# Performance work log

Hardware: AMD Instinct MI355X
Metric: run time of the kernel (lower is better)

Reference implementation:

```python
import jax, jax.numpy as jnp
import numpy as np

N, DIM = 4096, 1024

def setup_inputs() -> dict:
    key = jax.random.key(0)
    ks = jax.random.split(key, 5)
    scale = 1.0 / np.sqrt(DIM)
    return {
        "x": jax.random.normal(ks[0], (N, DIM), dtype=jnp.float32),
        "Wq": jax.random.normal(ks[1], (DIM, DIM), dtype=jnp.float32) * scale,
        "bq": jax.random.normal(ks[2], (DIM,), dtype=jnp.float32) * 0.01,
        "Wk": jax.random.normal(ks[3], (DIM, DIM), dtype=jnp.float32) * scale,
        "bk": jax.random.normal(ks[4], (DIM,), dtype=jnp.float32) * 0.01,
    }

def reference(x, Wq, bq, Wk, bk):
    # torch nn.Linear: y = x @ W.T + b
    q = x @ Wq.T + bq            # [N, D]
    k = x @ Wk.T + bk            # [N, D]
    scores = q @ k.T             # [N, N] (no 1/sqrt(d) scaling, as in source)
    attn = jax.nn.softmax(scores, axis=-1)
    return attn @ x              # weighted pooling over raw x (no value proj)
```

## Files before the change

### kernel.cpp

```cpp
#include <hip/hip_runtime.h>
#include <hip/hip_bf16.h>
#include <hip/hip_fp16.h>
#include <stdint.h>


using half8   = __attribute__((ext_vector_type(8))) _Float16;
using float4v = __attribute__((ext_vector_type(4))) float;
using int4v   = __attribute__((ext_vector_type(4))) int;
using uint2v  = __attribute__((ext_vector_type(2))) unsigned int;

#define QS        (6.0f / 32768.0f)
#define INV_S     (32768.0f / 6.0f)
#define INV_S256  (128.0f / 6.0f)
#define C_HH      (65536.0f * QS * QS)
#define C_X       (256.0f * QS * QS)

#define SX        (6.0f / 32768.0f)
#define SW        (0.25f / 32768.0f)
#define P_HH      (65536.0f * SX * SW)
#define P_X       (256.0f * SX * SW)

#define GLOAD_LDS16(gptr, ldsptr)                                              \
  __builtin_amdgcn_global_load_lds(                                            \
      (__attribute__((address_space(1))) void*)(uintptr_t)(gptr),              \
      (__attribute__((address_space(3))) void*)(unsigned)(uintptr_t)(ldsptr),  \
      16, 0, 0)

__device__ __forceinline__ void barrier_raw() {
  asm volatile("" ::: "memory");
  __builtin_amdgcn_s_barrier();
  asm volatile("" ::: "memory");
}

__device__ __forceinline__ int swz3(int row) {
  return (((row >> 2) & 3) << 1) ^ (row & 3);
}

__global__ __launch_bounds__(256, 2) void gemm_s_stats(
    const int8_t* __restrict__ Ahi, const int8_t* __restrict__ Alo,
    const int8_t* __restrict__ Bhi, const int8_t* __restrict__ Blo,
    _Float16* __restrict__ E, float2* __restrict__ stats)
{
  __shared__ __align__(16) int8_t smem[65536];
  int8_t* sAh = smem;
  int8_t* sAl = smem + 16384;
  int8_t* sBh = smem + 32768;
  int8_t* sBl = smem + 49152;

  const int tid  = threadIdx.x;
  const int wave = tid >> 6;
  const int lane = tid & 63;
  const int quad = lane >> 4;
  const int t16  = lane & 15;
  const int wm   = wave & 1;
  const int wn   = wave >> 1;
  const int row0 = blockIdx.y * 128;
  const int col0 = blockIdx.x * 128;

  const int seg  = lane & 3;
  const int rsub = lane >> 2;

  const int offA0 = (row0 + wave * 16 + rsub) * 2048 + seg * 16;
  const int offA1 = offA0 + 64 * 2048;
  const int offB0 = (col0 + wave * 16 + rsub) * 2048 + seg * 16;
  const int offB1 = offB0 + 64 * 2048;
  const int ldsT0 = (wave * 16) * 64;
  const int ldsT1 = (64 + wave * 16) * 64;

  int4v hh[4][4], cc[4][4];
#pragma unroll
  for (int i = 0; i < 4; ++i)
#pragma unroll
    for (int j = 0; j < 4; ++j) {
      hh[i][j] = (int4v){0, 0, 0, 0};
      cc[i][j] = (int4v){0, 0, 0, 0};
    }

  auto stage_AhBh = [&](int ks, int b) {
    const int k0 = ks * 64;
    GLOAD_LDS16(Ahi + offA0 + k0, sAh + b * 8192 + ldsT0);
    GLOAD_LDS16(Ahi + offA1 + k0, sAh + b * 8192 + ldsT1);
    GLOAD_LDS16(Bhi + offB0 + k0, sBh + b * 8192 + ldsT0);
    GLOAD_LDS16(Bhi + offB1 + k0, sBh + b * 8192 + ldsT1);
  };
  auto stage_Bl = [&](int ks, int b) {
    const int k0 = ks * 64;
    GLOAD_LDS16(Blo + offB0 + k0, sBl + b * 8192 + ldsT0);
    GLOAD_LDS16(Blo + offB1 + k0, sBl + b * 8192 + ldsT1);
  };
  auto stage_Al = [&](int ks, int b) {
    const int k0 = ks * 64;
    GLOAD_LDS16(Alo + offA0 + k0, sAl + b * 8192 + ldsT0);
    GLOAD_LDS16(Alo + offA1 + k0, sAl + b * 8192 + ldsT1);
  };

  stage_AhBh(0, 0);
  stage_Bl(0, 0);
  stage_Al(0, 0);

  int buf = 0;
  for (int ks = 0; ks < 16; ++ks) {
    asm volatile("s_waitcnt vmcnt(4)" ::: "memory");
    barrier_raw();
    if (ks < 15) stage_AhBh(ks + 1, buf ^ 1);

    int4v ah[4], bh[4];
#pragma unroll
    for (int i = 0; i < 4; ++i)
      ah[i] = *(const int4v*)(sAh + buf * 8192 +
                              (wm * 64 + i * 16 + t16) * 64 + quad * 16);
#pragma unroll
    for (int j = 0; j < 4; ++j)
      bh[j] = *(const int4v*)(sBh + buf * 8192 +
                              (wn * 64 + j * 16 + t16) * 64 + quad * 16);

    __builtin_amdgcn_s_setprio(1);
#pragma unroll
    for (int i = 0; i < 4; ++i)
#pragma unroll
      for (int j = 0; j < 4; ++j)
        hh[i][j] = __builtin_amdgcn_mfma_i32_16x16x64_i8(ah[i], bh[j], hh[i][j], 0, 0, 0);
    __builtin_amdgcn_s_setprio(0);

    if (ks < 15) asm volatile("s_waitcnt vmcnt(6)" ::: "memory");
    else         asm volatile("s_waitcnt vmcnt(2)" ::: "memory");
    barrier_raw();
    if (ks < 15) stage_Bl(ks + 1, buf ^ 1);

    int4v bl[4];
#pragma unroll
    for (int j = 0; j < 4; ++j)
      bl[j] = *(const int4v*)(sBl + buf * 8192 +
                              (wn * 64 + j * 16 + t16) * 64 + quad * 16);

    __builtin_amdgcn_s_setprio(1);
#pragma unroll
    for (int i = 0; i < 4; ++i)
#pragma unroll
      for (int j = 0; j < 4; ++j)
        cc[i][j] = __builtin_amdgcn_mfma_i32_16x16x64_i8(ah[i], bl[j], cc[i][j], 0, 0, 0);
    __builtin_amdgcn_s_setprio(0);

    if (ks < 15) asm volatile("s_waitcnt vmcnt(6)" ::: "memory");
    else         asm volatile("s_waitcnt vmcnt(0)" ::: "memory");
    barrier_raw();
    if (ks < 15) stage_Al(ks + 1, buf ^ 1);

    int4v al[4];
#pragma unroll
    for (int i = 0; i < 4; ++i)
      al[i] = *(const int4v*)(sAl + buf * 8192 +
                              (wm * 64 + i * 16 + t16) * 64 + quad * 16);

    __builtin_amdgcn_s_setprio(1);
#pragma unroll
    for (int i = 0; i < 4; ++i)
#pragma unroll
      for (int j = 0; j < 4; ++j)
        cc[i][j] = __builtin_amdgcn_mfma_i32_16x16x64_i8(al[i], bh[j], cc[i][j], 0, 0, 0);
    __builtin_amdgcn_s_setprio(0);

    buf ^= 1;
  }

  float* red = (float*)smem;

  float vv[4][4][4];
  float rmax[4][4];
#pragma unroll
  for (int i = 0; i < 4; ++i)
#pragma unroll
    for (int r = 0; r < 4; ++r) {
      float mx = -3.0e38f;
#pragma unroll
      for (int j = 0; j < 4; ++j) {
        float v = C_HH * (float)hh[i][j][r] + C_X * (float)cc[i][j][r];
        vv[i][j][r] = v;
        mx = fmaxf(mx, v);
      }
      mx = fmaxf(mx, __shfl_xor(mx, 1));
      mx = fmaxf(mx, __shfl_xor(mx, 2));
      mx = fmaxf(mx, __shfl_xor(mx, 4));
      mx = fmaxf(mx, __shfl_xor(mx, 8));
      rmax[i][r] = mx;
    }
  if (t16 == 0) {
#pragma unroll
    for (int i = 0; i < 4; ++i)
#pragma unroll
      for (int r = 0; r < 4; ++r)
        red[wn * 128 + wm * 64 + i * 16 + quad * 4 + r] = rmax[i][r];
  }
  __syncthreads();

  float mrow[4][4];
#pragma unroll
  for (int i = 0; i < 4; ++i)
#pragma unroll
    for (int r = 0; r < 4; ++r) {
      const int row = wm * 64 + i * 16 + quad * 4 + r;
      mrow[i][r] = fmaxf(red[row], red[128 + row]);
    }

  float rsum[4][4];
#pragma unroll
  for (int i = 0; i < 4; ++i)
#pragma unroll
    for (int r = 0; r < 4; ++r) {
      float s = 0.f;
#pragma unroll
      for (int j = 0; j < 4; ++j) {
        float e = __expf(vv[i][j][r] - mrow[i][r]);
        vv[i][j][r] = e;
        s += e;
      }
      s += __shfl_xor(s, 1);
      s += __shfl_xor(s, 2);
      s += __shfl_xor(s, 4);
      s += __shfl_xor(s, 8);
      rsum[i][r] = s;
    }
  if (t16 == 0) {
#pragma unroll
    for (int i = 0; i < 4; ++i)
#pragma unroll
      for (int r = 0; r < 4; ++r)
        red[256 + wn * 128 + wm * 64 + i * 16 + quad * 4 + r] = rsum[i][r];
  }

  uint16_t* img = (uint16_t*)(smem + 32768);
#pragma unroll
  for (int i = 0; i < 4; ++i)
#pragma unroll
    for (int j = 0; j < 4; ++j)
#pragma unroll
      for (int r = 0; r < 4; ++r) {
        const int row  = wm * 64 + i * 16 + quad * 4 + r;
        const int col  = wn * 64 + j * 16 + t16;
        const int colS = col ^ (((quad << 1) ^ r) << 3);
        _Float16 h = (_Float16)vv[i][j][r];
        img[row * 128 + colS] = *(const uint16_t*)&h;
      }
  __syncthreads();

#pragma unroll
  for (int it = 0; it < 8; ++it) {
    const int row    = wave * 32 + it * 4 + quad;
    const int chunkS = t16 ^ swz3(row);
    int4v v = *(const int4v*)&img[row * 128 + chunkS * 8];
    *(int4v*)&E[(size_t)(row0 + row) * 4096 + col0 + t16 * 8] = v;
  }

  if (wn == 0 && t16 == 0) {
#pragma unroll
    for (int i = 0; i < 4; ++i)
#pragma unroll
      for (int r = 0; r < 4; ++r) {
        const int row = wm * 64 + i * 16 + quad * 4 + r;
        const float l = red[256 + row] + red[256 + 128 + row];
        stats[(size_t)(row0 + row) * 32 + blockIdx.x] =
            make_float2(mrow[i][r], l);
      }
  }
}

__global__ __launch_bounds__(256, 2) void gemm_proj_i8(
    const int8_t* __restrict__ Ahi, const int8_t* __restrict__ Alo,
    const int8_t* __restrict__ Bhi, const int8_t* __restrict__ Blo,
    const float* __restrict__ biasQ, const float* __restrict__ biasK,
    int8_t* __restrict__ Ch, int8_t* __restrict__ Cl)
{
  __shared__ __align__(16) int8_t smem[65536];
  int8_t* sAh = smem;
  int8_t* sAl = smem + 16384;
  int8_t* sBh = smem + 32768;
  int8_t* sBl = smem + 49152;

  const int tid  = threadIdx.x;
  const int wave = tid >> 6;
  const int lane = tid & 63;
  const int quad = lane >> 4;
  const int t16  = lane & 15;
  const int wm   = wave & 1;
  const int wn   = wave >> 1;
  const int row0 = blockIdx.y * 128;
  const int col0 = blockIdx.x * 128;

  const int seg  = lane & 3;
  const int rsub = lane >> 2;

  const int offA0 = (row0 + wave * 16 + rsub) * 1024 + seg * 16;
  const int offA1 = offA0 + 64 * 1024;
  const int offB0 = (col0 + wave * 16 + rsub) * 1024 + seg * 16;
  const int offB1 = offB0 + 64 * 1024;
  const int ldsT0 = (wave * 16) * 64;
  const int ldsT1 = (64 + wave * 16) * 64;

  int4v hh[4][4], cc[4][4];
#pragma unroll
  for (int i = 0; i < 4; ++i)
#pragma unroll
    for (int j = 0; j < 4; ++j) {
      hh[i][j] = (int4v){0, 0, 0, 0};
      cc[i][j] = (int4v){0, 0, 0, 0};
    }

  auto stage_AhBh = [&](int ks, int b) {
    const int k0 = ks * 64;
    GLOAD_LDS16(Ahi + offA0 + k0, sAh + b * 8192 + ldsT0);
    GLOAD_LDS16(Ahi + offA1 + k0, sAh + b * 8192 + ldsT1);
    GLOAD_LDS16(Bhi + offB0 + k0, sBh + b * 8192 + ldsT0);
    GLOAD_LDS16(Bhi + offB1 + k0, sBh + b * 8192 + ldsT1);
  };
  auto stage_Bl = [&](int ks, int b) {
    const int k0 = ks * 64;
    GLOAD_LDS16(Blo + offB0 + k0, sBl + b * 8192 + ldsT0);
    GLOAD_LDS16(Blo + offB1 + k0, sBl + b * 8192 + ldsT1);
  };
  auto stage_Al = [&](int ks, int b) {
    const int k0 = ks * 64;
    GLOAD_LDS16(Alo + offA0 + k0, sAl + b * 8192 + ldsT0);
    GLOAD_LDS16(Alo + offA1 + k0, sAl + b * 8192 + ldsT1);
  };

  stage_AhBh(0, 0);
  stage_Bl(0, 0);
  stage_Al(0, 0);

  int buf = 0;
  for (int ks = 0; ks < 16; ++ks) {
    asm volatile("s_waitcnt vmcnt(4)" ::: "memory");
    barrier_raw();
    if (ks < 15) stage_AhBh(ks + 1, buf ^ 1);

    int4v ah[4], bh[4];
#pragma unroll
    for (int i = 0; i < 4; ++i)
      ah[i] = *(const int4v*)(sAh + buf * 8192 +
                              (wm * 64 + i * 16 + t16) * 64 + quad * 16);
#pragma unroll
    for (int j = 0; j < 4; ++j)
      bh[j] = *(const int4v*)(sBh + buf * 8192 +
                              (wn * 64 + j * 16 + t16) * 64 + quad * 16);

    __builtin_amdgcn_s_setprio(1);
#pragma unroll
    for (int i = 0; i < 4; ++i)
#pragma unroll
      for (int j = 0; j < 4; ++j)
        hh[i][j] = __builtin_amdgcn_mfma_i32_16x16x64_i8(ah[i], bh[j], hh[i][j], 0, 0, 0);
    __builtin_amdgcn_s_setprio(0);

    if (ks < 15) asm volatile("s_waitcnt vmcnt(6)" ::: "memory");
    else         asm volatile("s_waitcnt vmcnt(2)" ::: "memory");
    barrier_raw();
    if (ks < 15) stage_Bl(ks + 1, buf ^ 1);

    int4v bl[4];
#pragma unroll
    for (int j = 0; j < 4; ++j)
      bl[j] = *(const int4v*)(sBl + buf * 8192 +
                              (wn * 64 + j * 16 + t16) * 64 + quad * 16);

    __builtin_amdgcn_s_setprio(1);
#pragma unroll
    for (int i = 0; i < 4; ++i)
#pragma unroll
      for (int j = 0; j < 4; ++j)
        cc[i][j] = __builtin_amdgcn_mfma_i32_16x16x64_i8(ah[i], bl[j], cc[i][j], 0, 0, 0);
    __builtin_amdgcn_s_setprio(0);

    if (ks < 15) asm volatile("s_waitcnt vmcnt(6)" ::: "memory");
    else         asm volatile("s_waitcnt vmcnt(0)" ::: "memory");
    barrier_raw();
    if (ks < 15) stage_Al(ks + 1, buf ^ 1);

    int4v al[4];
#pragma unroll
    for (int i = 0; i < 4; ++i)
      al[i] = *(const int4v*)(sAl + buf * 8192 +
                              (wm * 64 + i * 16 + t16) * 64 + quad * 16);

    __builtin_amdgcn_s_setprio(1);
#pragma unroll
    for (int i = 0; i < 4; ++i)
#pragma unroll
      for (int j = 0; j < 4; ++j)
        cc[i][j] = __builtin_amdgcn_mfma_i32_16x16x64_i8(al[i], bh[j], cc[i][j], 0, 0, 0);
    __builtin_amdgcn_s_setprio(0);

    buf ^= 1;
  }

  uint16_t* img = (uint16_t*)(smem + 32768);
#pragma unroll
  for (int i = 0; i < 4; ++i) {
#pragma unroll
    for (int j = 0; j < 4; ++j) {
      const int ccol = col0 + wn * 64 + j * 16 + t16;
      const float* bp = (ccol < 1024) ? biasQ : (biasK - 1024);
#pragma unroll
      for (int r = 0; r < 4; ++r) {
        float v = P_HH * (float)hh[i][j][r] + P_X * (float)cc[i][j][r] + bp[ccol];
        int hi = (int)lrintf(v * INV_S256);
        hi = hi > 127 ? 127 : (hi < -127 ? -127 : hi);
        int lo = (int)lrintf(v * INV_S - 256.0f * (float)hi);
        lo = lo > 127 ? 127 : (lo < -127 ? -127 : lo);
        const int row  = wm * 64 + i * 16 + quad * 4 + r;
        const int col  = wn * 64 + j * 16 + t16;
        const int colS = col ^ (((quad << 1) ^ r) << 3);
        img[row * 128 + colS] = (uint16_t)((hi & 0xff) | ((lo & 0xff) << 8));
      }
    }
  }
  __syncthreads();

#pragma unroll
  for (int it = 0; it < 8; ++it) {
    const int row    = wave * 32 + it * 4 + quad;
    const int chunkS = t16 ^ swz3(row);
    int4v p = *(const int4v*)&img[row * 128 + chunkS * 8];
    const unsigned w0 = (unsigned)p[0], w1 = (unsigned)p[1];
    const unsigned w2 = (unsigned)p[2], w3 = (unsigned)p[3];
    uint2v hw, lw;
    hw[0] = (w0 & 0xffu) | (((w0 >> 16) & 0xffu) << 8) |
            ((w1 & 0xffu) << 16) | (((w1 >> 16) & 0xffu) << 24);
    hw[1] = (w2 & 0xffu) | (((w2 >> 16) & 0xffu) << 8) |
            ((w3 & 0xffu) << 16) | (((w3 >> 16) & 0xffu) << 24);
    lw[0] = ((w0 >> 8) & 0xffu) | (((w0 >> 24) & 0xffu) << 8) |
            (((w1 >> 8) & 0xffu) << 16) | ((w1 >> 24) << 24);
    lw[1] = ((w2 >> 8) & 0xffu) | (((w2 >> 24) & 0xffu) << 8) |
            (((w3 >> 8) & 0xffu) << 16) | ((w3 >> 24) << 24);
    const size_t go = (size_t)(row0 + row) * 2048 + col0 + t16 * 8;
    *(uint2v*)&Ch[go] = hw;
    *(uint2v*)&Cl[go] = lw;
  }
}

__global__ __launch_bounds__(512) void gemm_av(
    const uint16_t* __restrict__ E, const uint16_t* __restrict__ B,
    const float2* __restrict__ stats, float* __restrict__ out)
{
  __shared__ __align__(16) uint16_t stg[2][2][16384];
  __shared__ float betaS[128 * 33];

  const int L      = blockIdx.x;
  const int xcd    = L & 7;
  const int rest   = L >> 3;
  const int colb   = rest & 7;
  const int bandHi = rest >> 3;
  const int band   = xcd + 8 * bandHi;
  const int row0   = band * 128;
  const int col0   = colb * 128;

  const int tid  = threadIdx.x;
  const int wave = tid >> 6;
  const int z    = wave >> 2;
  const int gw   = wave & 3;
  const int lane = tid & 63;
  const int quad = lane >> 4;
  const int t16  = lane & 15;
  const int wm   = gw & 1;
  const int wn   = gw >> 1;

  const int c8   = lane & 7;
  const int r8   = lane >> 3;
  const int srcC = (c8 - r8) & 7;

  int offA[4], offB[4];
#pragma unroll
  for (int r = 0; r < 4; ++r) {
    offA[r] = (row0 + r * 32 + gw * 8 + r8) * 4096 + srcC * 8;
    offB[r] = (col0 + r * 32 + gw * 8 + r8) * 4096 + srcC * 8;
  }

  auto stage_s = [&](int s, int b) {
    const int k0h = (z * 16 + (s >> 1)) * 128 + (s & 1) * 64;
    uint16_t* sA = &stg[b][z][0];
    uint16_t* sB = &stg[b][z][8192];
#pragma unroll
    for (int r = 0; r < 4; ++r) {
      GLOAD_LDS16(E + offA[r] + k0h, &sA[(r * 32 + gw * 8) * 64]);
      GLOAD_LDS16(B + offB[r] + k0h, &sB[(r * 32 + gw * 8) * 64]);
    }
  };

  stage_s(0, 0);

  if (tid < 128) {
    const int row = row0 + tid;
    float2 st[32];
    float m = -3.0e38f;
#pragma unroll
    for (int t = 0; t < 32; ++t) {
      st[t] = stats[(size_t)row * 32 + t];
      m = fmaxf(m, st[t].x);
    }
    float l = 0.f;
#pragma unroll
    for (int t = 0; t < 32; ++t) l += st[t].y * __expf(st[t].x - m);
    const float inv = 1.0f / l;
#pragma unroll
    for (int t = 0; t < 32; ++t)
      betaS[tid * 33 + t] = __expf(st[t].x - m) * inv;
  }
  asm volatile("s_waitcnt vmcnt(0)" ::: "memory");
  __syncthreads();

  float4v acc[4][4];
#pragma unroll
  for (int i = 0; i < 4; ++i)
#pragma unroll
    for (int j = 0; j < 4; ++j)
      acc[i][j] = (float4v){0.f, 0.f, 0.f, 0.f};

  int buf = 0;
  for (int s = 0; s < 32; ++s) {
    if (s < 31) stage_s(s + 1, buf ^ 1);

    const int t = z * 16 + (s >> 1);
    _Float16 bb[4];
#pragma unroll
    for (int i = 0; i < 4; ++i)
      bb[i] = (_Float16)betaS[(wm * 64 + i * 16 + t16) * 33 + t];

    const uint16_t* sA = &stg[buf][z][0];
    const uint16_t* sB = &stg[buf][z][8192];

    half8 af[2][4], bf[2][4];
#pragma unroll
    for (int ks = 0; ks < 2; ++ks) {
#pragma unroll
      for (int i = 0; i < 4; ++i) {
        const int row = wm * 64 + i * 16 + t16;
        const int ch  = (ks * 4 + quad + (t16 & 7)) & 7;
        af[ks][i] = *(const half8*)&sA[row * 64 + ch * 8];
        half8 bs;
#pragma unroll
        for (int c = 0; c < 8; ++c) bs[c] = bb[i];
        af[ks][i] = af[ks][i] * bs;
      }
#pragma unroll
      for (int j = 0; j < 4; ++j) {
        const int row = wn * 64 + j * 16 + t16;
        const int ch  = (ks * 4 + quad + (t16 & 7)) & 7;
        bf[ks][j] = *(const half8*)&sB[row * 64 + ch * 8];
      }
    }

    __builtin_amdgcn_s_setprio(1);
#pragma unroll
    for (int ks = 0; ks < 2; ++ks)
#pragma unroll
      for (int i = 0; i < 4; ++i)
#pragma unroll
        for (int j = 0; j < 4; ++j)
          acc[i][j] = __builtin_amdgcn_mfma_f32_16x16x32_f16(af[ks][i], bf[ks][j], acc[i][j], 0, 0, 0);
    __builtin_amdgcn_s_setprio(0);

    if (s < 31) asm volatile("s_waitcnt vmcnt(0)" ::: "memory");
    barrier_raw();
    buf ^= 1;
  }

  float* xfer = (float*)stg;
#pragma unroll
  for (int h = 0; h < 2; ++h) {
    if (z == 1) {
#pragma unroll
      for (int i = 2 * h; i < 2 * h + 2; ++i)
#pragma unroll
        for (int j = 0; j < 4; ++j)
#pragma unroll
          for (int r = 0; r < 4; ++r) {
            const int e = (i - 2 * h) * 16 + j * 4 + r;
            xfer[e * 256 + gw * 64 + lane] = acc[i][j][r];
          }
    }
    __syncthreads();
    if (z == 0) {
#pragma unroll
      for (int i = 2 * h; i < 2 * h + 2; ++i)
#pragma unroll
        for (int j = 0; j < 4; ++j)
#pragma unroll
          for (int r = 0; r < 4; ++r) {
            const int e = (i - 2 * h) * 16 + j * 4 + r;
            acc[i][j][r] += xfer[e * 256 + gw * 64 + lane];
          }
    }
    __syncthreads();
  }

  float* img = (float*)((int8_t*)stg + 65536);
  if (z == 0) {
#pragma unroll
    for (int i = 0; i < 4; ++i)
#pragma unroll
      for (int j = 0; j < 4; ++j)
#pragma unroll
        for (int r = 0; r < 4; ++r) {
          const int row  = wm * 64 + i * 16 + quad * 4 + r;
          const int col  = wn * 64 + j * 16 + t16;
          const int colS = col ^ (((quad << 1) ^ r) << 2);
          img[row * 128 + colS] = acc[i][j][r];
        }
  }
  __syncthreads();

#pragma unroll
  for (int it = 0; it < 8; ++it) {
    const int row    = wave * 16 + (lane >> 2);
    const int chunk  = (lane & 3) * 8 + it;
    const int chunkS = chunk ^ swz3(row);
    float4v v = *(const float4v*)&img[row * 128 + chunkS * 4];
    *(float4v*)&out[(size_t)(row0 + row) * 1024 + col0 + chunk * 4] = v;
  }
}

__global__ __launch_bounds__(256) void quantT(
    const float* __restrict__ x, const float* __restrict__ Wq,
    const float* __restrict__ Wk,
    int8_t* __restrict__ xhi, int8_t* __restrict__ xlo,
    int8_t* __restrict__ whi, int8_t* __restrict__ wlo,
    uint16_t* __restrict__ xT)
{
  if (blockIdx.x < 6144) {
    int i = blockIdx.x * 256 + threadIdx.x;
    const float* src; int8_t* dh; int8_t* dl; int idx; float s256, s;
    if (i < 1048576)      { src = x;  idx = i;           dh = xhi; dl = xlo;
                            s256 = INV_S256; s = INV_S; }
    else if (i < 1310720) { src = Wq; idx = i - 1048576; dh = whi; dl = wlo;
                            s256 = 512.0f; s = 131072.0f; }
    else                  { src = Wk; idx = i - 1310720; dh = whi + 1048576;
                            dl = wlo + 1048576; s256 = 512.0f; s = 131072.0f; }
    float4 v = ((const float4*)src)[idx];
    float vv[4] = {v.x, v.y, v.z, v.w};
    int hp = 0, lp = 0;
#pragma unroll
    for (int c = 0; c < 4; ++c) {
      int h = (int)lrintf(vv[c] * s256);
      h = h > 127 ? 127 : (h < -127 ? -127 : h);
      int l = (int)lrintf(vv[c] * s - 256.0f * (float)h);
      l = l > 127 ? 127 : (l < -127 ? -127 : l);
      hp |= (h & 0xff) << (8 * c);
      lp |= (l & 0xff) << (8 * c);
    }
    ((int*)dh)[idx] = hp;
    ((int*)dl)[idx] = lp;
  } else {
    __shared__ float tile[32][33];
    const int tb = blockIdx.x - 6144;
    const int bx = tb & 31;
    const int by = tb >> 5;
    const int tx = threadIdx.x & 31;
    const int ty = threadIdx.x >> 5;
#pragma unroll
    for (int p = 0; p < 4; ++p) {
      const int row = by * 32 + ty + p * 8;
      tile[ty + p * 8][tx] = x[(size_t)row * 1024 + bx * 32 + tx];
    }
    __syncthreads();
#pragma unroll
    for (int p = 0; p < 4; ++p) {
      const int oc = ty + p * 8;
      __half hv = __float2half_rn(tile[tx][oc]);
      xT[(size_t)(bx * 32 + oc) * 4096 + by * 32 + tx] = *(uint16_t*)&hv;
    }
  }
}

extern "C" void kernel_launch(void* const* d_in, const int* in_sizes, int n_in,
                              void* d_out, int out_size, void* d_ws, size_t ws_size,
                              hipStream_t stream) {
  const int N = 4096, D = 1024;
  const float* x  = (const float*)d_in[0];
  const float* Wq = (const float*)d_in[1];
  const float* bq = (const float*)d_in[2];
  const float* Wk = (const float*)d_in[3];
  const float* bk = (const float*)d_in[4];
  float* out = (float*)d_out;

  char* w = (char*)d_ws;
  const size_t MiB = 1024 * 1024;
  int8_t*    xq_hi  = (int8_t*)   (w + 0  * MiB);
  int8_t*    xq_lo  = (int8_t*)   (w + 4  * MiB);
  int8_t*    Wqk_hi = (int8_t*)   (w + 8  * MiB);
  int8_t*    Wqk_lo = (int8_t*)   (w + 10 * MiB);
  int8_t*    qk_hi  = (int8_t*)   (w + 12 * MiB);
  int8_t*    qk_lo  = (int8_t*)   (w + 20 * MiB);
  _Float16*  E      = (_Float16*) (w + 36 * MiB);
  float2*    stats  = (float2*)   (w + 68 * MiB);
  uint16_t*  xTh    = (uint16_t*) (w + 72 * MiB);

  quantT<<<10240, 256, 0, stream>>>(x, Wq, Wk, xq_hi, xq_lo, Wqk_hi, Wqk_lo,
                                    xTh);

  gemm_proj_i8<<<dim3(2048 / 128, N / 128), 256, 0, stream>>>(
      xq_hi, xq_lo, Wqk_hi, Wqk_lo, bq, bk, qk_hi, qk_lo);

  gemm_s_stats<<<dim3(N / 128, N / 128), 256, 0, stream>>>(
      qk_hi, qk_lo, qk_hi + 1024, qk_lo + 1024, E, stats);

  gemm_av<<<256, 512, 0, stream>>>((const uint16_t*)E, xTh, stats, out);

  (void)in_sizes; (void)n_in; (void)out_size; (void)ws_size;
}
```

Baseline: 215.2 us.

## Replace split-K gemm_av with 128x64 tiles over 512 blocks of 256 threads

The attention-times-x GEMM drops its two-way split-K within a 512-thread block and instead uses 128x64 output tiles, giving 512 blocks of 256 threads with launch bounds allowing two blocks per CU. This removes the LDS cross-wave reduction and its extra barriers, and the smaller shared-memory footprint plus betaS stored as fp16 should let more blocks run at once. In exchange, each block reloads the full 128-row A strip for only 64 output columns, so global traffic for E roughly doubles, and the K loop is twice as long.

```diff
diff --git a/kernel.cpp b/kernel.cpp
--- a/kernel.cpp
+++ b/kernel.cpp
@@ -437,52 +437,52 @@
   }
 }
 
-__global__ __launch_bounds__(512) void gemm_av(
+__global__ __launch_bounds__(256, 2) void gemm_av(
     const uint16_t* __restrict__ E, const uint16_t* __restrict__ B,
     const float2* __restrict__ stats, float* __restrict__ out)
 {
-  __shared__ __align__(16) uint16_t stg[2][2][16384];
-  __shared__ float betaS[128 * 33];
+  __shared__ __align__(16) uint16_t stg[2][12288];
+  __shared__ _Float16 betaS[128 * 33];
 
   const int L      = blockIdx.x;
   const int xcd    = L & 7;
   const int rest   = L >> 3;
-  const int colb   = rest & 7;
-  const int bandHi = rest >> 3;
+  const int colb   = rest & 15;
+  const int bandHi = rest >> 4;
   const int band   = xcd + 8 * bandHi;
   const int row0   = band * 128;
-  const int col0   = colb * 128;
+  const int col0   = colb * 64;
 
   const int tid  = threadIdx.x;
   const int wave = tid >> 6;
-  const int z    = wave >> 2;
-  const int gw   = wave & 3;
   const int lane = tid & 63;
   const int quad = lane >> 4;
   const int t16  = lane & 15;
-  const int wm   = gw & 1;
-  const int wn   = gw >> 1;
-
+  const int wm   = wave & 1;
+  const int wn   = wave >> 1;
+
+  const int r8   = lane >> 3;
   const int c8   = lane & 7;
-  const int r8   = lane >> 3;
   const int srcC = (c8 - r8) & 7;
 
-  int offA[4], offB[4];
-#pragma unroll
-  for (int r = 0; r < 4; ++r) {
-    offA[r] = (row0 + r * 32 + gw * 8 + r8) * 4096 + srcC * 8;
-    offB[r] = (col0 + r * 32 + gw * 8 + r8) * 4096 + srcC * 8;
-  }
+  int offA[4], offBx[2];
+#pragma unroll
+  for (int p = 0; p < 4; ++p)
+    offA[p] = (row0 + p * 32 + wave * 8 + r8) * 4096 + srcC * 8;
+#pragma unroll
+  for (int p = 0; p < 2; ++p)
+    offBx[p] = (col0 + p * 32 + wave * 8 + r8) * 4096 + srcC * 8;
 
   auto stage_s = [&](int s, int b) {
-    const int k0h = (z * 16 + (s >> 1)) * 128 + (s & 1) * 64;
-    uint16_t* sA = &stg[b][z][0];
-    uint16_t* sB = &stg[b][z][8192];
-#pragma unroll
-    for (int r = 0; r < 4; ++r) {
-      GLOAD_LDS16(E + offA[r] + k0h, &sA[(r * 32 + gw * 8) * 64]);
-      GLOAD_LDS16(B + offB[r] + k0h, &sB[(r * 32 + gw * 8) * 64]);
-    }
+    const int k0h = s * 64;
+    uint16_t* sA = &stg[b][0];
+    uint16_t* sB = &stg[b][8192];
+#pragma unroll
+    for (int p = 0; p < 4; ++p)
+      GLOAD_LDS16(E + offA[p] + k0h, &sA[(p * 32 + wave * 8) * 64]);
+#pragma unroll
+    for (int p = 0; p < 2; ++p)
+      GLOAD_LDS16(B + offBx[p] + k0h, &sB[(p * 32 + wave * 8) * 64]);
   };
 
   stage_s(0, 0);
@@ -502,32 +502,32 @@
     const float inv = 1.0f / l;
 #pragma unroll
     for (int t = 0; t < 32; ++t)
-      betaS[tid * 33 + t] = __expf(st[t].x - m) * inv;
+      betaS[tid * 33 + t] = (_Float16)(__expf(st[t].x - m) * inv);
   }
   asm volatile("s_waitcnt vmcnt(0)" ::: "memory");
   __syncthreads();
 
-  float4v acc[4][4];
-#pragma unroll
-  for (int i = 0; i < 4; ++i)
-#pragma unroll
-    for (int j = 0; j < 4; ++j)
+  float4v acc[4][2];
+#pragma unroll
+  for (int i = 0; i < 4; ++i)
+#pragma unroll
+    for (int j = 0; j < 2; ++j)
       acc[i][j] = (float4v){0.f, 0.f, 0.f, 0.f};
 
   int buf = 0;
-  for (int s = 0; s < 32; ++s) {
-    if (s < 31) stage_s(s + 1, buf ^ 1);
-
-    const int t = z * 16 + (s >> 1);
+  for (int s = 0; s < 64; ++s) {
+    if (s < 63) stage_s(s + 1, buf ^ 1);
+
+    const int t = s >> 1;
     _Float16 bb[4];
 #pragma unroll
     for (int i = 0; i < 4; ++i)
-      bb[i] = (_Float16)betaS[(wm * 64 + i * 16 + t16) * 33 + t];
-
-    const uint16_t* sA = &stg[buf][z][0];
-    const uint16_t* sB = &stg[buf][z][8192];
-
-    half8 af[2][4], bf[2][4];
+      bb[i] = betaS[(wm * 64 + i * 16 + t16) * 33 + t];
+
+    const uint16_t* sA = &stg[buf][0];
+    const uint16_t* sB = &stg[buf][8192];
+
+    half8 af[2][4], bf[2][2];
 #pragma unroll
     for (int ks = 0; ks < 2; ++ks) {
 #pragma unroll
@@ -541,8 +541,8 @@
         af[ks][i] = af[ks][i] * bs;
       }
 #pragma unroll
-      for (int j = 0; j < 4; ++j) {
-        const int row = wn * 64 + j * 16 + t16;
+      for (int j = 0; j < 2; ++j) {
+        const int row = wn * 32 + j * 16 + t16;
         const int ch  = (ks * 4 + quad + (t16 & 7)) & 7;
         bf[ks][j] = *(const half8*)&sB[row * 64 + ch * 8];
       }
@@ -554,67 +554,35 @@
 #pragma unroll
       for (int i = 0; i < 4; ++i)
 #pragma unroll
-        for (int j = 0; j < 4; ++j)
+        for (int j = 0; j < 2; ++j)
           acc[i][j] = __builtin_amdgcn_mfma_f32_16x16x32_f16(af[ks][i], bf[ks][j], acc[i][j], 0, 0, 0);
     __builtin_amdgcn_s_setprio(0);
 
-    if (s < 31) asm volatile("s_waitcnt vmcnt(0)" ::: "memory");
+    if (s < 63) asm volatile("s_waitcnt vmcnt(0)" ::: "memory");
     barrier_raw();
     buf ^= 1;
   }
 
-  float* xfer = (float*)stg;
-#pragma unroll
-  for (int h = 0; h < 2; ++h) {
-    if (z == 1) {
-#pragma unroll
-      for (int i = 2 * h; i < 2 * h + 2; ++i)
-#pragma unroll
-        for (int j = 0; j < 4; ++j)
-#pragma unroll
-          for (int r = 0; r < 4; ++r) {
-            const int e = (i - 2 * h) * 16 + j * 4 + r;
-            xfer[e * 256 + gw * 64 + lane] = acc[i][j][r];
-          }
-    }
-    __syncthreads();
-    if (z == 0) {
-#pragma unroll
-      for (int i = 2 * h; i < 2 * h + 2; ++i)
-#pragma unroll
-        for (int j = 0; j < 4; ++j)
-#pragma unroll
-          for (int r = 0; r < 4; ++r) {
-            const int e = (i - 2 * h) * 16 + j * 4 + r;
-            acc[i][j][r] += xfer[e * 256 + gw * 64 + lane];
-          }
-    }
-    __syncthreads();
-  }
-
-  float* img = (float*)((int8_t*)stg + 65536);
-  if (z == 0) {
-#pragma unroll
-    for (int i = 0; i < 4; ++i)
-#pragma unroll
-      for (int j = 0; j < 4; ++j)
-#pragma unroll
-        for (int r = 0; r < 4; ++r) {
-          const int row  = wm * 64 + i * 16 + quad * 4 + r;
-          const int col  = wn * 64 + j * 16 + t16;
-          const int colS = col ^ (((quad << 1) ^ r) << 2);
-          img[row * 128 + colS] = acc[i][j][r];
-        }
-  }
+  float* img = (float*)stg;
+#pragma unroll
+  for (int i = 0; i < 4; ++i)
+#pragma unroll
+    for (int j = 0; j < 2; ++j)
+#pragma unroll
+      for (int r = 0; r < 4; ++r) {
+        const int row  = wm * 64 + i * 16 + quad * 4 + r;
+        const int col  = wn * 32 + j * 16 + t16;
+        const int colS = col ^ (swz3(row) << 2);
+        img[row * 64 + colS] = acc[i][j][r];
+      }
   __syncthreads();
 
 #pragma unroll
   for (int it = 0; it < 8; ++it) {
-    const int row    = wave * 16 + (lane >> 2);
-    const int chunk  = (lane & 3) * 8 + it;
-    const int chunkS = chunk ^ swz3(row);
-    float4v v = *(const float4v*)&img[row * 128 + chunkS * 4];
-    *(float4v*)&out[(size_t)(row0 + row) * 1024 + col0 + chunk * 4] = v;
+    const int row    = wave * 32 + it * 4 + quad;
+    const int chunkS = t16 ^ swz3(row);
+    float4v v = *(const float4v*)&img[row * 64 + chunkS * 4];
+    *(float4v*)&out[(size_t)(row0 + row) * 1024 + col0 + t16 * 4] = v;
   }
 }
 
@@ -702,7 +670,7 @@
   gemm_s_stats<<<dim3(N / 128, N / 128), 256, 0, stream>>>(
       qk_hi, qk_lo, qk_hi + 1024, qk_lo + 1024, E, stats);
 
-  gemm_av<<<256, 512, 0, stream>>>((const uint16_t*)E, xTh, stats, out);
+  gemm_av<<<512, 256, 0, stream>>>((const uint16_t*)E, xTh, stats, out);
 
   (void)in_sizes; (void)n_in; (void)out_size; (void)ws_size;
 }
```

Result: no change. 214.8 us (median of 2 runs) (-0.2%).
